# Kernel optimization log

Hardware: AMD Instinct MI355X
Metric: run time of the kernel (lower is better)

The kernel has to match this reference:

```python
import jax, jax.numpy as jnp
import numpy as np

N = 50000   # nodes
E = 800000  # edges (avg degree 16)
IN, H, OUT = 128, 256, 40


def setup_inputs() -> dict:
    key = jax.random.key(0)
    ks = jax.random.split(key, 7)
    x = jax.random.normal(ks[0], (N, IN), dtype=jnp.float32)
    edge_index = jax.random.randint(ks[1], (2, E), 0, N, dtype=jnp.int32)
    def w(k, fi, fo):
        return jax.random.normal(k, (fi, fo), dtype=jnp.float32) / np.sqrt(fi).astype(np.float32)
    return {
        "x": x,
        "edge_index": edge_index,
        "W0": w(ks[2], IN, H), "b0": jnp.zeros((H,), jnp.float32),
        "W1": w(ks[3], H, H),  "b1": jnp.zeros((H,), jnp.float32),
        "W2": w(ks[4], H, H),  "b2": jnp.zeros((H,), jnp.float32),
        "Wh": w(ks[5], H, OUT), "bh": jnp.zeros((OUT,), jnp.float32),
    }


def gcn_conv(x, src, dst, W, b, n):
    """PyG GCNConv: self-loops + symmetric D^-1/2 (A+I) D^-1/2 normalization."""
    h = x @ W  # [N, Fout]
    # degree with self-loop (edge weights are all 1)
    deg = jnp.ones((n,), h.dtype).at[dst].add(1.0)
    inv = jax.lax.rsqrt(deg)  # deg^{-1/2}
    coef = inv[src] * inv[dst]  # [E]
    agg = jax.ops.segment_sum(h[src] * coef[:, None], dst, num_segments=n)
    agg = agg + h * (inv * inv)[:, None]  # self-loop contribution
    return agg + b


def reference(x, edge_index, W0, b0, W1, b1, W2, b2, Wh, bh):
    src, dst = edge_index[0], edge_index[1]
    h = jax.nn.relu(gcn_conv(x, src, dst, W0, b0, N))   # conv0 + relu (dropout p=0)
    h = jax.nn.relu(gcn_conv(h, src, dst, W1, b1, N))   # conv1 + relu
    h = gcn_conv(h, src, dst, W2, b2, N)                # final conv (no relu)
    g = jnp.mean(h, axis=0, keepdims=True)              # batch=None -> global mean, [1, H]
    return g @ Wh + bh                                  # prediction head, [1, OUT]
```

## Files before the change

kernel.cpp:

```cpp
#include <hip/hip_runtime.h>

#define NN 50000
#define NE 800000
#define FIN 128
#define FH 256
#define FOUT 40
#define NPAD 50432
#define NN2 50048
#define NB 256
#define BSPAN 196
#define EBLK 4096
#define NBLK_A 196
#define NBLK_S 196

typedef float f32x4 __attribute__((ext_vector_type(4)));
typedef short bf16x8 __attribute__((ext_vector_type(8)));

__device__ __forceinline__ ushort f2bf(float f) {
    unsigned u = __float_as_uint(f);
    unsigned r = (u + 0x7FFFu + ((u >> 16) & 1u)) >> 16;
    return (ushort)r;
}
__device__ __forceinline__ float bf2f(ushort b) {
    return __uint_as_float(((unsigned)b) << 16);
}


__global__ __launch_bounds__(256) void bucket_cnt_kernel(const int* __restrict__ dst,
                                                         int* __restrict__ bcnt) {
    __shared__ int h[NB];
    const int t = threadIdx.x;
    h[t] = 0;
    __syncthreads();
    const int e0 = blockIdx.x * EBLK;
    const int n  = min(EBLK, NE - e0);
    for (int i = t; i < n; i += 256)
        atomicAdd(&h[dst[e0 + i] / BSPAN], 1);
    __syncthreads();
    if (h[t] > 0) atomicAdd(&bcnt[t], h[t]);
}

__global__ __launch_bounds__(256) void bucket_scan_kernel(const int* __restrict__ bcnt,
                                                          int* __restrict__ bbase,
                                                          int* __restrict__ bcur,
                                                          float* __restrict__ vbuf) {
    __shared__ int sh[256];
    int t = threadIdx.x;
    int v = bcnt[t];
    sh[t] = v;
    __syncthreads();
    #pragma unroll
    for (int off = 1; off < 256; off <<= 1) {
        int u = (t >= off) ? sh[t - off] : 0;
        __syncthreads();
        sh[t] += u;
        __syncthreads();
    }
    int excl = sh[t] - v;
    bbase[t] = excl;
    bcur[t]  = excl;
    if (t == 255) bbase[256] = sh[255];
    vbuf[t] = 0.0f;
}

__global__ __launch_bounds__(256) void binA_kernel(const int* __restrict__ src,
                                                   const int* __restrict__ dst,
                                                   int* __restrict__ bcur,
                                                   unsigned* __restrict__ inter) {
    __shared__ int hcnt[NB];
    __shared__ int hoff[NB];
    __shared__ int lcur[NB];
    __shared__ int gbase[NB];
    __shared__ unsigned stage[EBLK];

    const int t  = threadIdx.x;
    const int e0 = blockIdx.x * EBLK;
    const int n  = min(EBLK, NE - e0);

    hcnt[t] = 0;
    __syncthreads();
    for (int i = t; i < n; i += 256)
        atomicAdd(&hcnt[dst[e0 + i] / BSPAN], 1);
    __syncthreads();
    int v = hcnt[t];
    hoff[t] = v;
    __syncthreads();
    #pragma unroll
    for (int off = 1; off < NB; off <<= 1) {
        int u = (t >= off) ? hoff[t - off] : 0;
        __syncthreads();
        hoff[t] += u;
        __syncthreads();
    }
    int excl = hoff[t] - v;
    __syncthreads();
    hoff[t] = excl;
    lcur[t] = excl;
    if (v > 0) gbase[t] = atomicAdd(&bcur[t], v);
    __syncthreads();
    for (int i = t; i < n; i += 256) {
        int d = dst[e0 + i];
        int s = src[e0 + i];
        int b = d / BSPAN;
        int idx = atomicAdd(&lcur[b], 1);
        stage[idx] = ((unsigned)d << 16) | (unsigned)s;
    }
    __syncthreads();
    for (int i = t; i < n; i += 256) {
        unsigned rec = stage[i];
        int b = (int)(rec >> 16) / BSPAN;
        inter[gbase[b] + (i - hoff[b])] = rec;
    }
}

__global__ __launch_bounds__(256) void binB1_kernel(const unsigned* __restrict__ inter,
                                                    const int* __restrict__ bbase,
                                                    int* __restrict__ row_start,
                                                    float* __restrict__ inv,
                                                    float* __restrict__ wsum) {
    __shared__ int lcnt[BSPAN];
    __shared__ int sh[256];
    const int b   = blockIdx.x;
    const int nlo = b * BSPAN;
    const int nhi = min(nlo + BSPAN, NN);
    const int nn  = nhi - nlo;
    const int base = bbase[b];
    const int cnt  = bbase[b + 1] - base;
    const int t = threadIdx.x;

    for (int i = t; i < nn; i += 256) lcnt[i] = 0;
    __syncthreads();
    for (int i = t; i < cnt; i += 256)
        atomicAdd(&lcnt[(int)(inter[base + i] >> 16) - nlo], 1);
    __syncthreads();
    int c = (t < nn) ? lcnt[t] : 0;
    sh[t] = c;
    __syncthreads();
    #pragma unroll
    for (int off = 1; off < 256; off <<= 1) {
        int u = (t >= off) ? sh[t - off] : 0;
        __syncthreads();
        sh[t] += u;
        __syncthreads();
    }
    if (t < nn) {
        row_start[nlo + t] = base + sh[t] - c;
        inv[nlo + t]  = rsqrtf((float)(c + 1));
        wsum[nlo + t] = 0.0f;
    }
    if (b == NB - 1 && t == 0) row_start[NN] = NE;
}

__global__ __launch_bounds__(256) void binB2_kernel(const unsigned* __restrict__ inter,
                                                    const int* __restrict__ bbase,
                                                    const int* __restrict__ row_start,
                                                    const float* __restrict__ inv,
                                                    float2* __restrict__ edata,
                                                    float* __restrict__ wsum) {
    __shared__ int lcur[BSPAN];
    const int b   = blockIdx.x;
    const int nlo = b * BSPAN;
    const int nhi = min(nlo + BSPAN, NN);
    const int nn  = nhi - nlo;
    const int base = bbase[b];
    const int cnt  = bbase[b + 1] - base;
    const int t = threadIdx.x;

    for (int i = t; i < nn; i += 256) lcur[i] = row_start[nlo + i];
    __syncthreads();
    for (int i = t; i < cnt; i += 256) {
        unsigned rec = inter[base + i];
        int d = (int)(rec >> 16);
        int s = (int)(rec & 0xFFFFu);
        float coef = inv[s] * inv[d];
        int pos = atomicAdd(&lcur[d - nlo], 1);
        edata[pos] = make_float2(__int_as_float(s), coef);
        unsafeAtomicAdd(&wsum[s], coef);
    }
}


__global__ void wsplit_all_kernel(const float* __restrict__ W0, const float* __restrict__ W1,
                                  ushort* __restrict__ W0tH, ushort* __restrict__ W0tL,
                                  ushort* __restrict__ W1tH) {
    int idx = blockIdx.x * 256 + threadIdx.x;
    if (idx < FIN * FH) {
        int n = idx % FH;
        int k = idx / FH;
        float f = W0[idx];
        ushort h = f2bf(f);
        W0tH[n * FIN + k] = h;
        W0tL[n * FIN + k] = f2bf(f - bf2f(h));
    }
    int j = idx - FIN * FH;
    if (j >= 0 && j < FH * FH) {
        int n = j % FH;
        int k = j / FH;
        W1tH[n * FH + k] = f2bf(W1[j]);
    }
}


__global__ void xcvt_kernel(const float* __restrict__ x, ushort* __restrict__ xb) {
    int t = blockIdx.x * 256 + threadIdx.x;
    if (t >= NN2 * 32) return;
    int row = t >> 5;
    int c4  = t & 31;
    ushort4 o = make_ushort4(0, 0, 0, 0);
    if (row < NN) {
        float4 v = *reinterpret_cast<const float4*>(x + (size_t)row * FIN + c4 * 4);
        o = make_ushort4(f2bf(v.x), f2bf(v.y), f2bf(v.z), f2bf(v.w));
    }
    *reinterpret_cast<ushort4*>(xb + (size_t)row * FIN + c4 * 4) = o;
}


template<int TERMS, bool BIAS_RELU>
__global__ __launch_bounds__(256) void gemm_mfma_kernel(
    const ushort* __restrict__ AH, const ushort* __restrict__ AL,
    const ushort* __restrict__ BH, const ushort* __restrict__ BL,
    const float* __restrict__ bias,
    ushort* __restrict__ outB,
    int K) {
    constexpr int NARR = (TERMS == 3) ? 2 : 1;
    __shared__ ushort smem[(128 + 256) * 40 * NARR];
    ushort* Ah = smem;
    ushort* Bh = smem + 128 * 40;
    ushort* Al = (TERMS == 3) ? smem + 384 * 40 : nullptr;
    ushort* Bl = (TERMS == 3) ? smem + 384 * 40 + 128 * 40 : nullptr;

    const int tid  = threadIdx.x;
    const int lane = tid & 63;
    const int w    = tid >> 6;
    const int wr   = w >> 1;
    const int wc   = w & 1;
    const int row0 = blockIdx.x * 128;

    f32x4 acc[4][8] = {};

    for (int k0 = 0; k0 < K; k0 += 32) {
        #pragma unroll
        for (int i = 0; i < 2; ++i) {
            int c  = i * 256 + tid;
            int r  = c >> 2;
            int cb = c & 3;
            *reinterpret_cast<uint4*>(&Ah[r * 40 + cb * 8]) =
                *reinterpret_cast<const uint4*>(AH + (size_t)(row0 + r) * K + k0 + cb * 8);
            if (TERMS == 3)
                *reinterpret_cast<uint4*>(&Al[r * 40 + cb * 8]) =
                    *reinterpret_cast<const uint4*>(AL + (size_t)(row0 + r) * K + k0 + cb * 8);
        }
        #pragma unroll
        for (int i = 0; i < 4; ++i) {
            int c  = i * 256 + tid;
            int r  = c >> 2;
            int cb = c & 3;
            *reinterpret_cast<uint4*>(&Bh[r * 40 + cb * 8]) =
                *reinterpret_cast<const uint4*>(BH + (size_t)r * K + k0 + cb * 8);
            if (TERMS == 3)
                *reinterpret_cast<uint4*>(&Bl[r * 40 + cb * 8]) =
                    *reinterpret_cast<const uint4*>(BL + (size_t)r * K + k0 + cb * 8);
        }
        __syncthreads();

        const int rsel = lane & 15;
        const int ksel = (lane >> 4) * 8;
        bf16x8 ah[4], bh[8];
        #pragma unroll
        for (int m = 0; m < 4; ++m)
            ah[m] = *reinterpret_cast<const bf16x8*>(&Ah[(wr * 64 + m * 16 + rsel) * 40 + ksel]);
        #pragma unroll
        for (int n = 0; n < 8; ++n)
            bh[n] = *reinterpret_cast<const bf16x8*>(&Bh[(wc * 128 + n * 16 + rsel) * 40 + ksel]);

        if (TERMS == 3) {
            bf16x8 al[4], bl[8];
            #pragma unroll
            for (int m = 0; m < 4; ++m)
                al[m] = *reinterpret_cast<const bf16x8*>(&Al[(wr * 64 + m * 16 + rsel) * 40 + ksel]);
            #pragma unroll
            for (int n = 0; n < 8; ++n)
                bl[n] = *reinterpret_cast<const bf16x8*>(&Bl[(wc * 128 + n * 16 + rsel) * 40 + ksel]);
            #pragma unroll
            for (int m = 0; m < 4; ++m)
                #pragma unroll
                for (int n = 0; n < 8; ++n) {
                    acc[m][n] = __builtin_amdgcn_mfma_f32_16x16x32_bf16(ah[m], bh[n], acc[m][n], 0, 0, 0);
                    acc[m][n] = __builtin_amdgcn_mfma_f32_16x16x32_bf16(ah[m], bl[n], acc[m][n], 0, 0, 0);
                    acc[m][n] = __builtin_amdgcn_mfma_f32_16x16x32_bf16(al[m], bh[n], acc[m][n], 0, 0, 0);
                }
        } else {
            #pragma unroll
            for (int m = 0; m < 4; ++m)
                #pragma unroll
                for (int n = 0; n < 8; ++n)
                    acc[m][n] = __builtin_amdgcn_mfma_f32_16x16x32_bf16(ah[m], bh[n], acc[m][n], 0, 0, 0);
        }
        __syncthreads();
    }

    const int cl = lane & 15;
    const int rg = lane >> 4;
    float bn[8];
    if (BIAS_RELU) {
        #pragma unroll
        for (int n = 0; n < 8; ++n) bn[n] = bias[wc * 128 + n * 16 + cl];
    }
    #pragma unroll
    for (int m = 0; m < 4; ++m) {
        #pragma unroll
        for (int i = 0; i < 4; ++i) {
            int gr = row0 + wr * 64 + m * 16 + rg * 4 + i;
            #pragma unroll
            for (int n = 0; n < 8; ++n) {
                int gc = wc * 128 + n * 16 + cl;
                float o = acc[m][n][i];
                if (BIAS_RELU) o = fmaxf(o + bn[n], 0.0f);
                outB[(size_t)gr * FH + gc] = f2bf(o);
            }
        }
    }
}


__global__ __launch_bounds__(256) void gather_x_kernel(const ushort* __restrict__ xb,
                                                       const float2* __restrict__ edata,
                                                       const int* __restrict__ row_start,
                                                       const float* __restrict__ inv,
                                                       ushort* __restrict__ outH,
                                                       ushort* __restrict__ outL) {
    int node = blockIdx.x * 4 + (threadIdx.x >> 6);
    int lane = threadIdx.x & 63;
    if (node >= NN2) return;
    size_t o = (size_t)node * FIN + lane * 2;
    if (node >= NN) {
        *reinterpret_cast<ushort2*>(outH + o) = make_ushort2(0, 0);
        *reinterpret_cast<ushort2*>(outL + o) = make_ushort2(0, 0);
        return;
    }

    int beg = row_start[node];
    int end = row_start[node + 1];

    float iv = inv[node];
    float c  = iv * iv;
    ushort2 sv = *reinterpret_cast<const ushort2*>(xb + o);
    float2 a0 = make_float2(bf2f(sv.x) * c, bf2f(sv.y) * c);
    float2 a1 = make_float2(0.f, 0.f);
    float2 a2 = make_float2(0.f, 0.f);
    float2 a3 = make_float2(0.f, 0.f);

    int i = beg;
    if ((i & 1) && i < end) {
        float2 ed = edata[i];
        ushort2 u = *reinterpret_cast<const ushort2*>(xb + (size_t)__float_as_int(ed.x) * FIN + lane * 2);
        a0.x += bf2f(u.x) * ed.y; a0.y += bf2f(u.y) * ed.y;
        ++i;
    }
    for (; i + 8 <= end; i += 8) {
        float4 e01 = *reinterpret_cast<const float4*>(&edata[i]);
        float4 e23 = *reinterpret_cast<const float4*>(&edata[i + 2]);
        float4 e45 = *reinterpret_cast<const float4*>(&edata[i + 4]);
        float4 e67 = *reinterpret_cast<const float4*>(&edata[i + 6]);
        ushort2 u0 = *reinterpret_cast<const ushort2*>(xb + (size_t)__float_as_int(e01.x) * FIN + lane * 2);
        ushort2 u1 = *reinterpret_cast<const ushort2*>(xb + (size_t)__float_as_int(e01.z) * FIN + lane * 2);
        ushort2 u2 = *reinterpret_cast<const ushort2*>(xb + (size_t)__float_as_int(e23.x) * FIN + lane * 2);
        ushort2 u3 = *reinterpret_cast<const ushort2*>(xb + (size_t)__float_as_int(e23.z) * FIN + lane * 2);
        ushort2 u4 = *reinterpret_cast<const ushort2*>(xb + (size_t)__float_as_int(e45.x) * FIN + lane * 2);
        ushort2 u5 = *reinterpret_cast<const ushort2*>(xb + (size_t)__float_as_int(e45.z) * FIN + lane * 2);
        ushort2 u6 = *reinterpret_cast<const ushort2*>(xb + (size_t)__float_as_int(e67.x) * FIN + lane * 2);
        ushort2 u7 = *reinterpret_cast<const ushort2*>(xb + (size_t)__float_as_int(e67.z) * FIN + lane * 2);
        a0.x += bf2f(u0.x) * e01.y; a0.y += bf2f(u0.y) * e01.y;
        a1.x += bf2f(u1.x) * e01.w; a1.y += bf2f(u1.y) * e01.w;
        a2.x += bf2f(u2.x) * e23.y; a2.y += bf2f(u2.y) * e23.y;
        a3.x += bf2f(u3.x) * e23.w; a3.y += bf2f(u3.y) * e23.w;
        a0.x += bf2f(u4.x) * e45.y; a0.y += bf2f(u4.y) * e45.y;
        a1.x += bf2f(u5.x) * e45.w; a1.y += bf2f(u5.y) * e45.w;
        a2.x += bf2f(u6.x) * e67.y; a2.y += bf2f(u6.y) * e67.y;
        a3.x += bf2f(u7.x) * e67.w; a3.y += bf2f(u7.y) * e67.w;
    }
    for (; i + 2 <= end; i += 2) {
        float4 e01 = *reinterpret_cast<const float4*>(&edata[i]);
        ushort2 u0 = *reinterpret_cast<const ushort2*>(xb + (size_t)__float_as_int(e01.x) * FIN + lane * 2);
        ushort2 u1 = *reinterpret_cast<const ushort2*>(xb + (size_t)__float_as_int(e01.z) * FIN + lane * 2);
        a0.x += bf2f(u0.x) * e01.y; a0.y += bf2f(u0.y) * e01.y;
        a1.x += bf2f(u1.x) * e01.w; a1.y += bf2f(u1.y) * e01.w;
    }
    if (i < end) {
        float2 ed = edata[i];
        ushort2 u = *reinterpret_cast<const ushort2*>(xb + (size_t)__float_as_int(ed.x) * FIN + lane * 2);
        a0.x += bf2f(u.x) * ed.y; a0.y += bf2f(u.y) * ed.y;
    }

    float ax = a0.x + a1.x + a2.x + a3.x;
    float ay = a0.y + a1.y + a2.y + a3.y;
    ushort h0 = f2bf(ax), h1 = f2bf(ay);
    ushort l0 = f2bf(ax - bf2f(h0)), l1 = f2bf(ay - bf2f(h1));
    *reinterpret_cast<ushort2*>(outH + o) = make_ushort2(h0, h1);
    *reinterpret_cast<ushort2*>(outL + o) = make_ushort2(l0, l1);
}


__global__ __launch_bounds__(256) void gather_bf_kernel(const ushort* __restrict__ lin,
                                                        const float2* __restrict__ edata,
                                                        const int* __restrict__ row_start,
                                                        const float* __restrict__ inv,
                                                        const float* __restrict__ bias,
                                                        ushort* __restrict__ outB) {
    int node = blockIdx.x * 4 + (threadIdx.x >> 6);
    int lane = threadIdx.x & 63;
    if (node >= NN) return;

    int beg = row_start[node];
    int end = row_start[node + 1];

    float iv = inv[node];
    float c  = iv * iv;
    ushort4 sv = *reinterpret_cast<const ushort4*>(lin + (size_t)node * FH + lane * 4);
    float4 b = *reinterpret_cast<const float4*>(bias + lane * 4);
    float4 a0 = make_float4(bf2f(sv.x) * c + b.x, bf2f(sv.y) * c + b.y,
                            bf2f(sv.z) * c + b.z, bf2f(sv.w) * c + b.w);
    float4 a1 = make_float4(0.f, 0.f, 0.f, 0.f);
    float4 a2 = make_float4(0.f, 0.f, 0.f, 0.f);
    float4 a3 = make_float4(0.f, 0.f, 0.f, 0.f);

    int i = beg;
    if ((i & 1) && i < end) {
        float2 ed = edata[i];
        float cf = ed.y;
        ushort4 wv = *reinterpret_cast<const ushort4*>(lin + (size_t)__float_as_int(ed.x) * FH + lane * 4);
        a0.x += bf2f(wv.x) * cf; a0.y += bf2f(wv.y) * cf;
        a0.z += bf2f(wv.z) * cf; a0.w += bf2f(wv.w) * cf;
        ++i;
    }
    for (; i + 8 <= end; i += 8) {
        float4 e01 = *reinterpret_cast<const float4*>(&edata[i]);
        float4 e23 = *reinterpret_cast<const float4*>(&edata[i + 2]);
        float4 e45 = *reinterpret_cast<const float4*>(&edata[i + 4]);
        float4 e67 = *reinterpret_cast<const float4*>(&edata[i + 6]);
        ushort4 w0 = *reinterpret_cast<const ushort4*>(lin + (size_t)__float_as_int(e01.x) * FH + lane * 4);
        ushort4 w1 = *reinterpret_cast<const ushort4*>(lin + (size_t)__float_as_int(e01.z) * FH + lane * 4);
        ushort4 w2 = *reinterpret_cast<const ushort4*>(lin + (size_t)__float_as_int(e23.x) * FH + lane * 4);
        ushort4 w3 = *reinterpret_cast<const ushort4*>(lin + (size_t)__float_as_int(e23.z) * FH + lane * 4);
        ushort4 w4 = *reinterpret_cast<const ushort4*>(lin + (size_t)__float_as_int(e45.x) * FH + lane * 4);
        ushort4 w5 = *reinterpret_cast<const ushort4*>(lin + (size_t)__float_as_int(e45.z) * FH + lane * 4);
        ushort4 w6 = *reinterpret_cast<const ushort4*>(lin + (size_t)__float_as_int(e67.x) * FH + lane * 4);
        ushort4 w7 = *reinterpret_cast<const ushort4*>(lin + (size_t)__float_as_int(e67.z) * FH + lane * 4);
        a0.x += bf2f(w0.x) * e01.y; a0.y += bf2f(w0.y) * e01.y;
        a0.z += bf2f(w0.z) * e01.y; a0.w += bf2f(w0.w) * e01.y;
        a1.x += bf2f(w1.x) * e01.w; a1.y += bf2f(w1.y) * e01.w;
        a1.z += bf2f(w1.z) * e01.w; a1.w += bf2f(w1.w) * e01.w;
        a2.x += bf2f(w2.x) * e23.y; a2.y += bf2f(w2.y) * e23.y;
        a2.z += bf2f(w2.z) * e23.y; a2.w += bf2f(w2.w) * e23.y;
        a3.x += bf2f(w3.x) * e23.w; a3.y += bf2f(w3.y) * e23.w;
        a3.z += bf2f(w3.z) * e23.w; a3.w += bf2f(w3.w) * e23.w;
        a0.x += bf2f(w4.x) * e45.y; a0.y += bf2f(w4.y) * e45.y;
        a0.z += bf2f(w4.z) * e45.y; a0.w += bf2f(w4.w) * e45.y;
        a1.x += bf2f(w5.x) * e45.w; a1.y += bf2f(w5.y) * e45.w;
        a1.z += bf2f(w5.z) * e45.w; a1.w += bf2f(w5.w) * e45.w;
        a2.x += bf2f(w6.x) * e67.y; a2.y += bf2f(w6.y) * e67.y;
        a2.z += bf2f(w6.z) * e67.y; a2.w += bf2f(w6.w) * e67.y;
        a3.x += bf2f(w7.x) * e67.w; a3.y += bf2f(w7.y) * e67.w;
        a3.z += bf2f(w7.z) * e67.w; a3.w += bf2f(w7.w) * e67.w;
    }
    for (; i + 2 <= end; i += 2) {
        float4 e01 = *reinterpret_cast<const float4*>(&edata[i]);
        ushort4 w0 = *reinterpret_cast<const ushort4*>(lin + (size_t)__float_as_int(e01.x) * FH + lane * 4);
        ushort4 w1 = *reinterpret_cast<const ushort4*>(lin + (size_t)__float_as_int(e01.z) * FH + lane * 4);
        a0.x += bf2f(w0.x) * e01.y; a0.y += bf2f(w0.y) * e01.y;
        a0.z += bf2f(w0.z) * e01.y; a0.w += bf2f(w0.w) * e01.y;
        a1.x += bf2f(w1.x) * e01.w; a1.y += bf2f(w1.y) * e01.w;
        a1.z += bf2f(w1.z) * e01.w; a1.w += bf2f(w1.w) * e01.w;
    }
    if (i < end) {
        float2 ed = edata[i];
        float cf = ed.y;
        ushort4 wv = *reinterpret_cast<const ushort4*>(lin + (size_t)__float_as_int(ed.x) * FH + lane * 4);
        a0.x += bf2f(wv.x) * cf; a0.y += bf2f(wv.y) * cf;
        a0.z += bf2f(wv.z) * cf; a0.w += bf2f(wv.w) * cf;
    }

    float4 acc = make_float4(a0.x + a1.x + a2.x + a3.x,
                             a0.y + a1.y + a2.y + a3.y,
                             a0.z + a1.z + a2.z + a3.z,
                             a0.w + a1.w + a2.w + a3.w);

    float r0 = fmaxf(acc.x, 0.f), r1 = fmaxf(acc.y, 0.f);
    float r2 = fmaxf(acc.z, 0.f), r3 = fmaxf(acc.w, 0.f);
    *reinterpret_cast<ushort4*>(outB + (size_t)node * FH + lane * 4) =
        make_ushort4(f2bf(r0), f2bf(r1), f2bf(r2), f2bf(r3));
}


__global__ __launch_bounds__(256) void colsumw_kernel(const ushort* __restrict__ a1,
                                                      const float* __restrict__ wsum,
                                                      const float* __restrict__ inv,
                                                      float* __restrict__ v) {
    __shared__ float sh[4][256];
    int wid  = threadIdx.x >> 6;
    int lane = threadIdx.x & 63;
    int r0 = blockIdx.x * 256;
    int r1 = r0 + 256; if (r1 > NN) r1 = NN;

    float4 acc = make_float4(0.f, 0.f, 0.f, 0.f);
    for (int r = r0 + wid; r < r1; r += 4) {
        float iv = inv[r];
        float wr = wsum[r] + iv * iv;
        ushort4 u = *reinterpret_cast<const ushort4*>(a1 + (size_t)r * FH + lane * 4);
        acc.x += bf2f(u.x) * wr;
        acc.y += bf2f(u.y) * wr;
        acc.z += bf2f(u.z) * wr;
        acc.w += bf2f(u.w) * wr;
    }
    *reinterpret_cast<float4*>(&sh[wid][lane * 4]) = acc;
    __syncthreads();
    if (wid == 0) {
        float4 s1 = *reinterpret_cast<const float4*>(&sh[1][lane * 4]);
        float4 s2 = *reinterpret_cast<const float4*>(&sh[2][lane * 4]);
        float4 s3 = *reinterpret_cast<const float4*>(&sh[3][lane * 4]);
        unsafeAtomicAdd(&v[lane * 4 + 0], acc.x + s1.x + s2.x + s3.x);
        unsafeAtomicAdd(&v[lane * 4 + 1], acc.y + s1.y + s2.y + s3.y);
        unsafeAtomicAdd(&v[lane * 4 + 2], acc.z + s1.z + s2.z + s3.z);
        unsafeAtomicAdd(&v[lane * 4 + 3], acc.w + s1.w + s2.w + s3.w);
    }
}

__global__ __launch_bounds__(256) void head2_kernel(const float* __restrict__ v,
                                                    const float* __restrict__ W2,
                                                    const float* __restrict__ b2,
                                                    const float* __restrict__ Wh,
                                                    const float* __restrict__ bh,
                                                    float* __restrict__ out) {
    __shared__ float m[FH];
    int t = threadIdx.x;
    const float scale = 1.0f / (float)NN;
    float s = 0.0f;
    for (int f = 0; f < FH; ++f)
        s += v[f] * W2[f * FH + t];
    m[t] = s * scale + b2[t];
    __syncthreads();
    if (t < FOUT) {
        float o = 0.0f;
        for (int f = 0; f < FH; ++f)
            o += m[f] * Wh[f * FOUT + t];
        out[t] = o + bh[t];
    }
}


extern "C" void kernel_launch(void* const* d_in, const int* in_sizes, int n_in,
                              void* d_out, int out_size, void* d_ws, size_t ws_size,
                              hipStream_t stream) {
    const float* x   = (const float*)d_in[0];
    const int*   ei  = (const int*)d_in[1];
    const float* W0  = (const float*)d_in[2];
    const float* b0  = (const float*)d_in[3];
    const float* W1  = (const float*)d_in[4];
    const float* b1  = (const float*)d_in[5];
    const float* W2  = (const float*)d_in[6];
    const float* b2  = (const float*)d_in[7];
    const float* Wh  = (const float*)d_in[8];
    const float* bh  = (const float*)d_in[9];
    float* out = (float*)d_out;

    const int* src = ei;
    const int* dst = ei + NE;

    float*    inv       = (float*)d_ws;
    int*      row_start = (int*)(inv + NPAD);
    float*    wsum      = (float*)(row_start + NPAD);
    int*      bcnt      = (int*)(wsum + NPAD);
    int*      bbase     = bcnt + 256;
    int*      bcur      = bbase + 320;
    float*    vbuf      = (float*)(bcur + 256);
    unsigned* inter     = (unsigned*)(vbuf + 256);
    float2*   edata     = (float2*)(inter + NE);
    ushort*   W0tH      = (ushort*)(edata + NE);
    ushort*   W0tL      = W0tH + 256 * 128;
    ushort*   W1tH      = W0tL + 256 * 128;
    ushort*   xb        = W1tH + 256 * 256;
    ushort*   aggxH     = xb + (size_t)NN2 * 128;
    ushort*   aggxL     = aggxH + (size_t)NN2 * 128;
    ushort*   linb      = aggxH;
    ushort*   h0H       = aggxL + (size_t)NN2 * 128;
    ushort*   a1H       = h0H;

    const int gemm_grid = NN2 / 128;
    const int nblk_gx = NN2 / 4;
    const int nblk_g  = (NN + 3) / 4;

    hipMemsetAsync(bcnt, 0, NB * sizeof(int), stream);
    bucket_cnt_kernel<<<NBLK_A, 256, 0, stream>>>(dst, bcnt);
    bucket_scan_kernel<<<1, 256, 0, stream>>>(bcnt, bbase, bcur, vbuf);
    binA_kernel<<<NBLK_A, 256, 0, stream>>>(src, dst, bcur, inter);
    binB1_kernel<<<NB, 256, 0, stream>>>(inter, bbase, row_start, inv, wsum);
    binB2_kernel<<<NB, 256, 0, stream>>>(inter, bbase, row_start, inv, edata, wsum);
    wsplit_all_kernel<<<(FIN * FH + FH * FH + 255) / 256, 256, 0, stream>>>(W0, W1, W0tH, W0tL, W1tH);
    xcvt_kernel<<<(NN2 * 32 + 255) / 256, 256, 0, stream>>>(x, xb);

    gather_x_kernel<<<nblk_gx, 256, 0, stream>>>(xb, edata, row_start, inv, aggxH, aggxL);
    gemm_mfma_kernel<3, true><<<gemm_grid, 256, 0, stream>>>(aggxH, aggxL, W0tH, W0tL, b0,
                                                             h0H, FIN);

    gemm_mfma_kernel<1, false><<<gemm_grid, 256, 0, stream>>>(h0H, nullptr, W1tH, nullptr, nullptr,
                                                              linb, FH);
    gather_bf_kernel<<<nblk_g, 256, 0, stream>>>(linb, edata, row_start, inv, b1, a1H);

    colsumw_kernel<<<NBLK_S, 256, 0, stream>>>(a1H, wsum, inv, vbuf);
    head2_kernel<<<1, 256, 0, stream>>>(vbuf, W2, b2, Wh, bh, out);
}
```

Baseline: 300.6 us.

## Fuse layer-1 gather with weighted column sum; merge weight and x conversion kernels

Merges the layer-1 neighbour gather (bias+ReLU) with the weighted column-sum reduction into one persistent grid-stride kernel. Each wave accumulates the per-node contribution directly into registers, so the bf16 activation matrix is never written or re-read. The gather unroll drops from 8 to 4 edges with alignment peeling. It also fuses the weight split/transposition and x bf16 conversion into a single launch. This removes the round trip through global memory and two launches, at the cost of fewer in-flight loads per wave and a fixed 1024-block grid.

```diff
diff --git a/kernel.cpp b/kernel.cpp
--- a/kernel.cpp
+++ b/kernel.cpp
@@ -11,7 +11,7 @@
 #define BSPAN 196
 #define EBLK 4096
 #define NBLK_A 196
-#define NBLK_S 196
+#define GBLK 1024
 
 typedef float f32x4 __attribute__((ext_vector_type(4)));
 typedef short bf16x8 __attribute__((ext_vector_type(8)));
@@ -180,38 +180,34 @@
 }
 
 
-__global__ void wsplit_all_kernel(const float* __restrict__ W0, const float* __restrict__ W1,
-                                  ushort* __restrict__ W0tH, ushort* __restrict__ W0tL,
-                                  ushort* __restrict__ W1tH) {
-    int idx = blockIdx.x * 256 + threadIdx.x;
-    if (idx < FIN * FH) {
-        int n = idx % FH;
-        int k = idx / FH;
-        float f = W0[idx];
+__global__ void prep_kernel(const float* __restrict__ W0, const float* __restrict__ W1,
+                            const float* __restrict__ x,
+                            ushort* __restrict__ W0tH, ushort* __restrict__ W0tL,
+                            ushort* __restrict__ W1tH, ushort* __restrict__ xb) {
+    int t = blockIdx.x * 256 + threadIdx.x;
+    if (t < NN2 * 32) {
+        int row = t >> 5;
+        int c4  = t & 31;
+        ushort4 o = make_ushort4(0, 0, 0, 0);
+        if (row < NN) {
+            float4 v = *reinterpret_cast<const float4*>(x + (size_t)row * FIN + c4 * 4);
+            o = make_ushort4(f2bf(v.x), f2bf(v.y), f2bf(v.z), f2bf(v.w));
+        }
+        *reinterpret_cast<ushort4*>(xb + (size_t)row * FIN + c4 * 4) = o;
+    }
+    if (t < FIN * FH) {
+        int n = t % FH;
+        int k = t / FH;
+        float f = W0[t];
         ushort h = f2bf(f);
         W0tH[n * FIN + k] = h;
         W0tL[n * FIN + k] = f2bf(f - bf2f(h));
-    }
-    int j = idx - FIN * FH;
-    if (j >= 0 && j < FH * FH) {
+    } else if (t < FIN * FH + FH * FH) {
+        int j = t - FIN * FH;
         int n = j % FH;
         int k = j / FH;
         W1tH[n * FH + k] = f2bf(W1[j]);
     }
-}
-
-
-__global__ void xcvt_kernel(const float* __restrict__ x, ushort* __restrict__ xb) {
-    int t = blockIdx.x * 256 + threadIdx.x;
-    if (t >= NN2 * 32) return;
-    int row = t >> 5;
-    int c4  = t & 31;
-    ushort4 o = make_ushort4(0, 0, 0, 0);
-    if (row < NN) {
-        float4 v = *reinterpret_cast<const float4*>(x + (size_t)row * FIN + c4 * 4);
-        o = make_ushort4(f2bf(v.x), f2bf(v.y), f2bf(v.z), f2bf(v.w));
-    }
-    *reinterpret_cast<ushort4*>(xb + (size_t)row * FIN + c4 * 4) = o;
 }
 
 
@@ -401,127 +397,84 @@
 }
 
 
-__global__ __launch_bounds__(256) void gather_bf_kernel(const ushort* __restrict__ lin,
-                                                        const float2* __restrict__ edata,
-                                                        const int* __restrict__ row_start,
-                                                        const float* __restrict__ inv,
-                                                        const float* __restrict__ bias,
-                                                        ushort* __restrict__ outB) {
-    int node = blockIdx.x * 4 + (threadIdx.x >> 6);
-    int lane = threadIdx.x & 63;
-    if (node >= NN) return;
-
-    int beg = row_start[node];
-    int end = row_start[node + 1];
-
-    float iv = inv[node];
-    float c  = iv * iv;
-    ushort4 sv = *reinterpret_cast<const ushort4*>(lin + (size_t)node * FH + lane * 4);
-    float4 b = *reinterpret_cast<const float4*>(bias + lane * 4);
-    float4 a0 = make_float4(bf2f(sv.x) * c + b.x, bf2f(sv.y) * c + b.y,
-                            bf2f(sv.z) * c + b.z, bf2f(sv.w) * c + b.w);
-    float4 a1 = make_float4(0.f, 0.f, 0.f, 0.f);
-    float4 a2 = make_float4(0.f, 0.f, 0.f, 0.f);
-    float4 a3 = make_float4(0.f, 0.f, 0.f, 0.f);
-
-    int i = beg;
-    if ((i & 1) && i < end) {
-        float2 ed = edata[i];
-        float cf = ed.y;
-        ushort4 wv = *reinterpret_cast<const ushort4*>(lin + (size_t)__float_as_int(ed.x) * FH + lane * 4);
-        a0.x += bf2f(wv.x) * cf; a0.y += bf2f(wv.y) * cf;
-        a0.z += bf2f(wv.z) * cf; a0.w += bf2f(wv.w) * cf;
-        ++i;
-    }
-    for (; i + 8 <= end; i += 8) {
-        float4 e01 = *reinterpret_cast<const float4*>(&edata[i]);
-        float4 e23 = *reinterpret_cast<const float4*>(&edata[i + 2]);
-        float4 e45 = *reinterpret_cast<const float4*>(&edata[i + 4]);
-        float4 e67 = *reinterpret_cast<const float4*>(&edata[i + 6]);
-        ushort4 w0 = *reinterpret_cast<const ushort4*>(lin + (size_t)__float_as_int(e01.x) * FH + lane * 4);
-        ushort4 w1 = *reinterpret_cast<const ushort4*>(lin + (size_t)__float_as_int(e01.z) * FH + lane * 4);
-        ushort4 w2 = *reinterpret_cast<const ushort4*>(lin + (size_t)__float_as_int(e23.x) * FH + lane * 4);
-        ushort4 w3 = *reinterpret_cast<const ushort4*>(lin + (size_t)__float_as_int(e23.z) * FH + lane * 4);
-        ushort4 w4 = *reinterpret_cast<const ushort4*>(lin + (size_t)__float_as_int(e45.x) * FH + lane * 4);
-        ushort4 w5 = *reinterpret_cast<const ushort4*>(lin + (size_t)__float_as_int(e45.z) * FH + lane * 4);
-        ushort4 w6 = *reinterpret_cast<const ushort4*>(lin + (size_t)__float_as_int(e67.x) * FH + lane * 4);
-        ushort4 w7 = *reinterpret_cast<const ushort4*>(lin + (size_t)__float_as_int(e67.z) * FH + lane * 4);
-        a0.x += bf2f(w0.x) * e01.y; a0.y += bf2f(w0.y) * e01.y;
-        a0.z += bf2f(w0.z) * e01.y; a0.w += bf2f(w0.w) * e01.y;
-        a1.x += bf2f(w1.x) * e01.w; a1.y += bf2f(w1.y) * e01.w;
-        a1.z += bf2f(w1.z) * e01.w; a1.w += bf2f(w1.w) * e01.w;
-        a2.x += bf2f(w2.x) * e23.y; a2.y += bf2f(w2.y) * e23.y;
-        a2.z += bf2f(w2.z) * e23.y; a2.w += bf2f(w2.w) * e23.y;
-        a3.x += bf2f(w3.x) * e23.w; a3.y += bf2f(w3.y) * e23.w;
-        a3.z += bf2f(w3.z) * e23.w; a3.w += bf2f(w3.w) * e23.w;
-        a0.x += bf2f(w4.x) * e45.y; a0.y += bf2f(w4.y) * e45.y;
-        a0.z += bf2f(w4.z) * e45.y; a0.w += bf2f(w4.w) * e45.y;
-        a1.x += bf2f(w5.x) * e45.w; a1.y += bf2f(w5.y) * e45.w;
-        a1.z += bf2f(w5.z) * e45.w; a1.w += bf2f(w5.w) * e45.w;
-        a2.x += bf2f(w6.x) * e67.y; a2.y += bf2f(w6.y) * e67.y;
-        a2.z += bf2f(w6.z) * e67.y; a2.w += bf2f(w6.w) * e67.y;
-        a3.x += bf2f(w7.x) * e67.w; a3.y += bf2f(w7.y) * e67.w;
-        a3.z += bf2f(w7.z) * e67.w; a3.w += bf2f(w7.w) * e67.w;
-    }
-    for (; i + 2 <= end; i += 2) {
-        float4 e01 = *reinterpret_cast<const float4*>(&edata[i]);
-        ushort4 w0 = *reinterpret_cast<const ushort4*>(lin + (size_t)__float_as_int(e01.x) * FH + lane * 4);
-        ushort4 w1 = *reinterpret_cast<const ushort4*>(lin + (size_t)__float_as_int(e01.z) * FH + lane * 4);
-        a0.x += bf2f(w0.x) * e01.y; a0.y += bf2f(w0.y) * e01.y;
-        a0.z += bf2f(w0.z) * e01.y; a0.w += bf2f(w0.w) * e01.y;
-        a1.x += bf2f(w1.x) * e01.w; a1.y += bf2f(w1.y) * e01.w;
-        a1.z += bf2f(w1.z) * e01.w; a1.w += bf2f(w1.w) * e01.w;
-    }
-    if (i < end) {
-        float2 ed = edata[i];
-        float cf = ed.y;
-        ushort4 wv = *reinterpret_cast<const ushort4*>(lin + (size_t)__float_as_int(ed.x) * FH + lane * 4);
-        a0.x += bf2f(wv.x) * cf; a0.y += bf2f(wv.y) * cf;
-        a0.z += bf2f(wv.z) * cf; a0.w += bf2f(wv.w) * cf;
-    }
-
-    float4 acc = make_float4(a0.x + a1.x + a2.x + a3.x,
-                             a0.y + a1.y + a2.y + a3.y,
-                             a0.z + a1.z + a2.z + a3.z,
-                             a0.w + a1.w + a2.w + a3.w);
-
-    float r0 = fmaxf(acc.x, 0.f), r1 = fmaxf(acc.y, 0.f);
-    float r2 = fmaxf(acc.z, 0.f), r3 = fmaxf(acc.w, 0.f);
-    *reinterpret_cast<ushort4*>(outB + (size_t)node * FH + lane * 4) =
-        make_ushort4(f2bf(r0), f2bf(r1), f2bf(r2), f2bf(r3));
-}
-
-
-__global__ __launch_bounds__(256) void colsumw_kernel(const ushort* __restrict__ a1,
-                                                      const float* __restrict__ wsum,
-                                                      const float* __restrict__ inv,
-                                                      float* __restrict__ v) {
+__global__ __launch_bounds__(256) void gather_colsum_kernel(const ushort* __restrict__ lin,
+                                                            const float2* __restrict__ edata,
+                                                            const int* __restrict__ row_start,
+                                                            const float* __restrict__ inv,
+                                                            const float* __restrict__ wsum,
+                                                            const float* __restrict__ bias,
+                                                            float* __restrict__ v) {
     __shared__ float sh[4][256];
-    int wid  = threadIdx.x >> 6;
-    int lane = threadIdx.x & 63;
-    int r0 = blockIdx.x * 256;
-    int r1 = r0 + 256; if (r1 > NN) r1 = NN;
-
-    float4 acc = make_float4(0.f, 0.f, 0.f, 0.f);
-    for (int r = r0 + wid; r < r1; r += 4) {
-        float iv = inv[r];
-        float wr = wsum[r] + iv * iv;
-        ushort4 u = *reinterpret_cast<const ushort4*>(a1 + (size_t)r * FH + lane * 4);
-        acc.x += bf2f(u.x) * wr;
-        acc.y += bf2f(u.y) * wr;
-        acc.z += bf2f(u.z) * wr;
-        acc.w += bf2f(u.w) * wr;
-    }
-    *reinterpret_cast<float4*>(&sh[wid][lane * 4]) = acc;
+    const int wid  = threadIdx.x >> 6;
+    const int lane = threadIdx.x & 63;
+    const float4 b = *reinterpret_cast<const float4*>(bias + lane * 4);
+
+    float4 vp = make_float4(0.f, 0.f, 0.f, 0.f);
+
+    for (int node = blockIdx.x * 4 + wid; node < NN; node += GBLK * 4) {
+        int beg = row_start[node];
+        int end = row_start[node + 1];
+
+        float iv = inv[node];
+        float c  = iv * iv;
+        ushort4 sv = *reinterpret_cast<const ushort4*>(lin + (size_t)node * FH + lane * 4);
+        float4 a0 = make_float4(bf2f(sv.x) * c + b.x, bf2f(sv.y) * c + b.y,
+                                bf2f(sv.z) * c + b.z, bf2f(sv.w) * c + b.w);
+        float4 a1 = make_float4(0.f, 0.f, 0.f, 0.f);
+        float4 a2 = make_float4(0.f, 0.f, 0.f, 0.f);
+        float4 a3 = make_float4(0.f, 0.f, 0.f, 0.f);
+
+        int i = beg;
+        int pre = (4 - (beg & 3)) & 3;
+        int pe = beg + pre; if (pe > end) pe = end;
+        for (; i < pe; ++i) {
+            float2 ed = edata[i];
+            float cf = ed.y;
+            ushort4 wv = *reinterpret_cast<const ushort4*>(lin + (size_t)__float_as_int(ed.x) * FH + lane * 4);
+            a0.x += bf2f(wv.x) * cf; a0.y += bf2f(wv.y) * cf;
+            a0.z += bf2f(wv.z) * cf; a0.w += bf2f(wv.w) * cf;
+        }
+        for (; i + 4 <= end; i += 4) {
+            float4 e01 = *reinterpret_cast<const float4*>(&edata[i]);
+            float4 e23 = *reinterpret_cast<const float4*>(&edata[i + 2]);
+            ushort4 w0 = *reinterpret_cast<const ushort4*>(lin + (size_t)__float_as_int(e01.x) * FH + lane * 4);
+            ushort4 w1 = *reinterpret_cast<const ushort4*>(lin + (size_t)__float_as_int(e01.z) * FH + lane * 4);
+            ushort4 w2 = *reinterpret_cast<const ushort4*>(lin + (size_t)__float_as_int(e23.x) * FH + lane * 4);
+            ushort4 w3 = *reinterpret_cast<const ushort4*>(lin + (size_t)__float_as_int(e23.z) * FH + lane * 4);
+            a0.x += bf2f(w0.x) * e01.y; a0.y += bf2f(w0.y) * e01.y;
+            a0.z += bf2f(w0.z) * e01.y; a0.w += bf2f(w0.w) * e01.y;
+            a1.x += bf2f(w1.x) * e01.w; a1.y += bf2f(w1.y) * e01.w;
+            a1.z += bf2f(w1.z) * e01.w; a1.w += bf2f(w1.w) * e01.w;
+            a2.x += bf2f(w2.x) * e23.y; a2.y += bf2f(w2.y) * e23.y;
+            a2.z += bf2f(w2.z) * e23.y; a2.w += bf2f(w2.w) * e23.y;
+            a3.x += bf2f(w3.x) * e23.w; a3.y += bf2f(w3.y) * e23.w;
+            a3.z += bf2f(w3.z) * e23.w; a3.w += bf2f(w3.w) * e23.w;
+        }
+        for (; i < end; ++i) {
+            float2 ed = edata[i];
+            float cf = ed.y;
+            ushort4 wv = *reinterpret_cast<const ushort4*>(lin + (size_t)__float_as_int(ed.x) * FH + lane * 4);
+            a0.x += bf2f(wv.x) * cf; a0.y += bf2f(wv.y) * cf;
+            a0.z += bf2f(wv.z) * cf; a0.w += bf2f(wv.w) * cf;
+        }
+
+        float wn = wsum[node] + c;
+        vp.x += fmaxf(a0.x + a1.x + a2.x + a3.x, 0.f) * wn;
+        vp.y += fmaxf(a0.y + a1.y + a2.y + a3.y, 0.f) * wn;
+        vp.z += fmaxf(a0.z + a1.z + a2.z + a3.z, 0.f) * wn;
+        vp.w += fmaxf(a0.w + a1.w + a2.w + a3.w, 0.f) * wn;
+    }
+
+    *reinterpret_cast<float4*>(&sh[wid][lane * 4]) = vp;
     __syncthreads();
     if (wid == 0) {
         float4 s1 = *reinterpret_cast<const float4*>(&sh[1][lane * 4]);
         float4 s2 = *reinterpret_cast<const float4*>(&sh[2][lane * 4]);
         float4 s3 = *reinterpret_cast<const float4*>(&sh[3][lane * 4]);
-        unsafeAtomicAdd(&v[lane * 4 + 0], acc.x + s1.x + s2.x + s3.x);
-        unsafeAtomicAdd(&v[lane * 4 + 1], acc.y + s1.y + s2.y + s3.y);
-        unsafeAtomicAdd(&v[lane * 4 + 2], acc.z + s1.z + s2.z + s3.z);
-        unsafeAtomicAdd(&v[lane * 4 + 3], acc.w + s1.w + s2.w + s3.w);
+        unsafeAtomicAdd(&v[lane * 4 + 0], vp.x + s1.x + s2.x + s3.x);
+        unsafeAtomicAdd(&v[lane * 4 + 1], vp.y + s1.y + s2.y + s3.y);
+        unsafeAtomicAdd(&v[lane * 4 + 2], vp.z + s1.z + s2.z + s3.z);
+        unsafeAtomicAdd(&v[lane * 4 + 3], vp.w + s1.w + s2.w + s3.w);
     }
 }
 
@@ -583,11 +536,9 @@
     ushort*   aggxL     = aggxH + (size_t)NN2 * 128;
     ushort*   linb      = aggxH;
     ushort*   h0H       = aggxL + (size_t)NN2 * 128;
-    ushort*   a1H       = h0H;
 
     const int gemm_grid = NN2 / 128;
     const int nblk_gx = NN2 / 4;
-    const int nblk_g  = (NN + 3) / 4;
 
     hipMemsetAsync(bcnt, 0, NB * sizeof(int), stream);
     bucket_cnt_kernel<<<NBLK_A, 256, 0, stream>>>(dst, bcnt);
@@ -595,8 +546,7 @@
     binA_kernel<<<NBLK_A, 256, 0, stream>>>(src, dst, bcur, inter);
     binB1_kernel<<<NB, 256, 0, stream>>>(inter, bbase, row_start, inv, wsum);
     binB2_kernel<<<NB, 256, 0, stream>>>(inter, bbase, row_start, inv, edata, wsum);
-    wsplit_all_kernel<<<(FIN * FH + FH * FH + 255) / 256, 256, 0, stream>>>(W0, W1, W0tH, W0tL, W1tH);
-    xcvt_kernel<<<(NN2 * 32 + 255) / 256, 256, 0, stream>>>(x, xb);
+    prep_kernel<<<(NN2 * 32 + 255) / 256, 256, 0, stream>>>(W0, W1, x, W0tH, W0tL, W1tH, xb);
 
     gather_x_kernel<<<nblk_gx, 256, 0, stream>>>(xb, edata, row_start, inv, aggxH, aggxL);
     gemm_mfma_kernel<3, true><<<gemm_grid, 256, 0, stream>>>(aggxH, aggxL, W0tH, W0tL, b0,
@@ -604,8 +554,8 @@
 
     gemm_mfma_kernel<1, false><<<gemm_grid, 256, 0, stream>>>(h0H, nullptr, W1tH, nullptr, nullptr,
                                                               linb, FH);
-    gather_bf_kernel<<<nblk_g, 256, 0, stream>>>(linb, edata, row_start, inv, b1, a1H);
-
-    colsumw_kernel<<<NBLK_S, 256, 0, stream>>>(a1H, wsum, inv, vbuf);
+
+    gather_colsum_kernel<<<GBLK, 256, 0, stream>>>(linb, edata, row_start, inv, wsum, b1, vbuf);
+
     head2_kernel<<<1, 256, 0, stream>>>(vbuf, W2, b2, Wh, bh, out);
 }
```

Measured after the change: 365.7 us. +21.6%, slower.
